# Optimization experiments

Measured on AMD Instinct MI355X. Metric: run time of the kernel, lower is better.

## Reference

```python
import jax, jax.numpy as jnp
import numpy as np


def setup_inputs() -> dict:
    key = jax.random.key(0)
    k1, k2, k3 = jax.random.split(key, 3)
    early = jax.random.normal(k1, (64, 1, 512, 512), dtype=jnp.float32)
    middle = jax.random.normal(k2, (64, 1, 256, 256), dtype=jnp.float32)
    deep = jax.random.normal(k3, (64, 1, 128, 128), dtype=jnp.float32)
    return {"early": early, "middle": middle, "deep": deep, "max_features": 500000}


def reference(early, middle, deep, max_features):
    # Concatenate all scores and find the threshold = (max_features)-th entry of
    # the descending sort, i.e. the (max_features+1)-th largest value.
    all_scores = jnp.concatenate([early.ravel(), middle.ravel(), deep.ravel()])
    n = all_scores.shape[0]
    if max_features >= n:
        thresh = jnp.asarray(0.0, dtype=all_scores.dtype)
    else:
        # top_k(k+1)[-1] == sort(descending)[k]; avoids a full sort.
        topk_vals, _ = jax.lax.top_k(all_scores, max_features + 1)
        thresh = topk_vals[-1]
    thresh = jax.lax.stop_gradient(thresh)
    early_out = jnp.where(early < thresh, jnp.zeros((), early.dtype), early)
    middle_out = jnp.where(middle < thresh, jnp.zeros((), middle.dtype), middle)
    deep_out = jnp.where(deep < thresh, jnp.zeros((), deep.dtype), deep)
    return (early_out, middle_out, deep_out)
```

## Files before the change

kernel.cpp:

```cpp
#include <hip/hip_runtime.h>

typedef float nfloat4 __attribute__((ext_vector_type(4)));

#define WS_CANDCNT 0
#define WS_B1      1
#define WS_K2      2
#define WS_PFX     3
#define WS_K3      4
#define H1_REP     32
#define H2_REP     8
#define WS_HIST1R  16
#define WS_HIST2R  (16 + H1_REP * 256)
#define WS_HIST3   (WS_HIST2R + H2_REP * 4096)
#define WS_ZEND    (WS_HIST3 + 4096)
#define WS_CAND    WS_ZEND

#define STASH 2048

__device__ __forceinline__ unsigned fkey(float f) {
  unsigned x = __float_as_uint(f);
  return x ^ ((x & 0x80000000u) ? 0xFFFFFFFFu : 0x80000000u);
}
__device__ __forceinline__ float unkey(unsigned u) {
  unsigned x = u ^ ((u & 0x80000000u) ? 0x80000000u : 0xFFFFFFFFu);
  return __uint_as_float(x);
}

__device__ __forceinline__ unsigned block_scan_incl(unsigned v, unsigned* sh4) {
  const int t = threadIdx.x;
  unsigned p = v;
#pragma unroll
  for (int off = 1; off < 64; off <<= 1) {
    unsigned y = __shfl_up(p, off);
    if ((t & 63) >= off) p += y;
  }
  if ((t & 63) == 63) sh4[t >> 6] = p;
  __syncthreads();
  unsigned wo = 0;
  for (int w = 0; w < (t >> 6); ++w) wo += sh4[w];
  __syncthreads();
  return p + wo;
}

__device__ __forceinline__ uint2 select_desc256(const unsigned* __restrict__ gh,
                                                unsigned k, unsigned* sh4, unsigned* sel2) {
  const int t = threadIdx.x;
  unsigned cnt = gh[255 - t];
  unsigned incl = block_scan_incl(cnt, sh4);
  unsigned excl = incl - cnt;
  if (excl < k && incl >= k) { sel2[0] = (unsigned)(255 - t); sel2[1] = k - excl; }
  __syncthreads();
  uint2 r; r.x = sel2[0]; r.y = sel2[1];
  __syncthreads();
  return r;
}

__device__ __forceinline__ uint2 select_desc4096(const unsigned* __restrict__ gh,
                                                 unsigned k, unsigned* sh4, unsigned* sel2) {
  const int t = threadIdx.x;
  unsigned loc[16]; unsigned s = 0;
  const int base = 4095 - t * 16;
#pragma unroll
  for (int j = 0; j < 16; ++j) { unsigned c = gh[base - j]; loc[j] = c; s += c; }
  unsigned incl = block_scan_incl(s, sh4);
  unsigned excl = incl - s;
  if (excl < k && incl >= k) {
    unsigned cum = excl; int j = 0;
    while (cum + loc[j] < k) { cum += loc[j]; ++j; }
    sel2[0] = (unsigned)(base - j); sel2[1] = k - cum;
  }
  __syncthreads();
  uint2 r; r.x = sel2[0]; r.y = sel2[1];
  __syncthreads();
  return r;
}

__global__ void zero_ws(unsigned* __restrict__ ws) {
  int i = blockIdx.x * blockDim.x + threadIdx.x;
  if (i < WS_ZEND) ws[i] = 0u;
}

__global__ void __launch_bounds__(1024) hist1_kernel(
    const float* __restrict__ e, const float* __restrict__ m,
    const float* __restrict__ d, int n0v, int n1v, int n2v,
    unsigned* __restrict__ ws) {
  __shared__ unsigned h[256 * 32];
  for (int i = threadIdx.x; i < 256 * 32; i += 1024) h[i] = 0u;
  __syncthreads();
  const unsigned sub = threadIdx.x & 31u;
  const int gid = blockIdx.x * 1024 + threadIdx.x;
  const int G = gridDim.x * 1024;

  auto acc1 = [&](float4 f) {
    atomicAdd(&h[((fkey(f.x) >> 24) << 5) | sub], 1u);
    atomicAdd(&h[((fkey(f.y) >> 24) << 5) | sub], 1u);
    atomicAdd(&h[((fkey(f.z) >> 24) << 5) | sub], 1u);
    atomicAdd(&h[((fkey(f.w) >> 24) << 5) | sub], 1u);
  };
  auto sweep = [&](const float* src, int nv) {
    const float4* a4 = (const float4*)src;
    int v = gid;
    for (; v + 3 * G < nv; v += 4 * G) {
      float4 f0 = a4[v]; float4 f1 = a4[v + G];
      float4 f2 = a4[v + 2 * G]; float4 f3 = a4[v + 3 * G];
      acc1(f0); acc1(f1); acc1(f2); acc1(f3);
    }
    for (; v < nv; v += G) acc1(a4[v]);
  };
  sweep(e, n0v); sweep(m, n1v); sweep(d, n2v);
  __syncthreads();
  const int t = threadIdx.x;
  if (t < 256) {
    unsigned s = 0;
#pragma unroll
    for (int j = 0; j < 32; ++j) s += h[(t << 5) + ((t + j) & 31)];
    if (s) atomicAdd(&ws[WS_HIST1R + (blockIdx.x & (H1_REP - 1)) * 256 + t], s);
  }
}

__global__ void __launch_bounds__(256) sel1_kernel(
    const int* __restrict__ maxf, unsigned* __restrict__ ws, long long n) {
  __shared__ unsigned h256[256];
  __shared__ unsigned sh4[4];
  __shared__ unsigned sel2[2];
  const int t = threadIdx.x;
  unsigned s = 0;
#pragma unroll
  for (int r = 0; r < H1_REP; ++r) s += ws[WS_HIST1R + r * 256 + t];
  h256[t] = s;
  __syncthreads();
  long long kk = (long long)maxf[0] + 1;
  if (kk > n) {
    if (t == 0) ws[WS_B1] = 0x80u;
    return;
  }
  uint2 r = select_desc256(h256, (unsigned)kk, sh4, sel2);
  if (t == 0) { ws[WS_B1] = r.x; ws[WS_K2] = r.y; }
}

__global__ void __launch_bounds__(1024) scatter_kernel(
    const float* __restrict__ e, const float* __restrict__ m, const float* __restrict__ d,
    float* __restrict__ out, unsigned* __restrict__ ws, unsigned cap,
    int e_blks, int m_blks) {
  const int t = threadIdx.x;
  const int bid = blockIdx.x;
  __shared__ float    sh_v[STASH];
  __shared__ unsigned sh_i[STASH];
  __shared__ unsigned sh_cnt;
  __shared__ unsigned sh_base;
  if (t == 0) sh_cnt = 0u;
  const unsigned b1 = ws[WS_B1];
  __syncthreads();
  const float4* in4;
  if (bid < e_blks)               in4 = (const float4*)e + (long long)bid * 2048;
  else if (bid < e_blks + m_blks) in4 = (const float4*)m + (long long)(bid - e_blks) * 2048;
  else                            in4 = (const float4*)d + (long long)(bid - e_blks - m_blks) * 2048;
  const int out_base_v = bid * 2048;
  nfloat4* out4 = (nfloat4*)out + out_base_v;
  float* gcV = (float*)(ws + WS_CAND);
  unsigned* gcI = ws + WS_CAND + cap;
  auto emit1 = [&](float4 f, int v) {
    unsigned kx = fkey(f.x), ky = fkey(f.y), kz = fkey(f.z), kw = fkey(f.w);
    nfloat4 o;
    o.x = ((kx >> 24) >= b1) ? f.x : 0.0f;
    o.y = ((ky >> 24) >= b1) ? f.y : 0.0f;
    o.z = ((kz >> 24) >= b1) ? f.z : 0.0f;
    o.w = ((kw >> 24) >= b1) ? f.w : 0.0f;
    __builtin_nontemporal_store(o, &out4[v]);
    unsigned ks[4] = {kx, ky, kz, kw};
    float fs[4] = {f.x, f.y, f.z, f.w};
#pragma unroll
    for (int cc = 0; cc < 4; ++cc) {
      if ((ks[cc] >> 24) == b1) {
        unsigned idx = (unsigned)(out_base_v + v) * 4u + (unsigned)cc;
        unsigned pos = atomicAdd(&sh_cnt, 1u);
        if (pos < STASH) { sh_v[pos] = fs[cc]; sh_i[pos] = idx; }
        else {
          unsigned g = atomicAdd(&ws[WS_CANDCNT], 1u);
          gcV[g] = fs[cc]; gcI[g] = idx;
        }
      }
    }
  };
  float4 f0 = in4[t];
  float4 f1 = in4[1024 + t];
  emit1(f0, t);
  emit1(f1, 1024 + t);
  __syncthreads();
  if (t == 0) {
    unsigned tot = sh_cnt < STASH ? sh_cnt : STASH;
    sh_base = tot ? atomicAdd(&ws[WS_CANDCNT], tot) : 0u;
    sh_cnt = tot;
  }
  __syncthreads();
  const unsigned tot = sh_cnt;
  const unsigned base = sh_base;
  for (unsigned i = t; i < tot; i += 1024) {
    gcV[base + i] = sh_v[i];
    gcI[base + i] = sh_i[i];
  }
}

__global__ void __launch_bounds__(256) candhist2_kernel(
    unsigned* __restrict__ ws, unsigned cap) {
  const int t = threadIdx.x;
  __shared__ unsigned sh_hist[4096];
  for (int i = t; i < 4096; i += 256) sh_hist[i] = 0u;
  __syncthreads();
  unsigned cnt = ws[WS_CANDCNT]; if (cnt > cap) cnt = cap;
  const float* candV = (const float*)(ws + WS_CAND);
  const unsigned G = gridDim.x * 256;
  for (unsigned i = blockIdx.x * 256 + t; i < cnt; i += G) {
    unsigned u = fkey(candV[i]);
    atomicAdd(&sh_hist[(u >> 12) & 0xFFFu], 1u);
  }
  __syncthreads();
  const unsigned rep = (blockIdx.x & (H2_REP - 1)) * 4096u;
  for (int i = t; i < 4096; i += 256) {
    unsigned v = sh_hist[i];
    if (v) atomicAdd(&ws[WS_HIST2R + rep + i], v);
  }
}

__global__ void __launch_bounds__(256) candhist3_kernel(
    const int* __restrict__ maxf, unsigned* __restrict__ ws, unsigned cap, long long n) {
  const int t = threadIdx.x;
  __shared__ unsigned sh_hist[4096];
  __shared__ unsigned sh4[4];
  __shared__ unsigned sel2[2];

  long long kk = (long long)maxf[0] + 1;
  unsigned pfx;
  if (kk > n) {
    pfx = 0x80u << 12;
  } else {
    for (int i = t; i < 4096; i += 256) {
      unsigned s = 0;
#pragma unroll
      for (int r = 0; r < H2_REP; ++r) s += ws[WS_HIST2R + r * 4096 + i];
      sh_hist[i] = s;
    }
    __syncthreads();
    unsigned b1 = ws[WS_B1];
    unsigned k2 = ws[WS_K2];
    uint2 r2 = select_desc4096(sh_hist, k2, sh4, sel2);
    pfx = (b1 << 12) | r2.x;
    if (blockIdx.x == 0 && t == 0) { ws[WS_PFX] = pfx; ws[WS_K3] = r2.y; }
    __syncthreads();
  }
  for (int i = t; i < 4096; i += 256) sh_hist[i] = 0u;
  __syncthreads();

  unsigned cnt = ws[WS_CANDCNT]; if (cnt > cap) cnt = cap;
  const float* candV = (const float*)(ws + WS_CAND);
  const unsigned G = gridDim.x * 256;
  for (unsigned i = blockIdx.x * 256 + t; i < cnt; i += G) {
    unsigned u = fkey(candV[i]);
    if ((u >> 12) == pfx) atomicAdd(&sh_hist[u & 0xFFFu], 1u);
  }
  __syncthreads();
  for (int i = t; i < 4096; i += 256) {
    unsigned v = sh_hist[i];
    if (v) atomicAdd(&ws[WS_HIST3 + i], v);
  }
}

__global__ void __launch_bounds__(256) fixup_kernel(
    float* __restrict__ out, const int* __restrict__ maxf,
    unsigned* __restrict__ ws, unsigned cap, long long n) {
  const int t = threadIdx.x;
  __shared__ unsigned sh4[4];
  __shared__ unsigned sel2[2];

  long long kk = (long long)maxf[0] + 1;
  float th;
  if (kk > n) {
    th = 0.0f;
    __syncthreads();
  } else {
    unsigned pfx = ws[WS_PFX];
    unsigned k3  = ws[WS_K3];
    uint2 r3 = select_desc4096(ws + WS_HIST3, k3, sh4, sel2);
    th = unkey((pfx << 12) | r3.x);
  }

  unsigned cnt = ws[WS_CANDCNT]; if (cnt > cap) cnt = cap;
  const float* candV = (const float*)(ws + WS_CAND);
  const unsigned* candI = ws + WS_CAND + cap;
  const unsigned G = gridDim.x * 256;
  for (unsigned i = blockIdx.x * 256 + t; i < cnt; i += G) {
    float f = candV[i];
    if (f < th) out[candI[i]] = 0.0f;
  }
}

extern "C" void kernel_launch(void* const* d_in, const int* in_sizes, int n_in,
                              void* d_out, int out_size, void* d_ws, size_t ws_size,
                              hipStream_t stream) {
  const float* e = (const float*)d_in[0];
  const float* m = (const float*)d_in[1];
  const float* d = (const float*)d_in[2];
  const int* maxf = (const int*)d_in[3];
  float* out = (float*)d_out;
  unsigned* ws = (unsigned*)d_ws;

  const long long n0 = in_sizes[0], n1 = in_sizes[1], n2 = in_sizes[2];
  const long long n = n0 + n1 + n2;
  const int n0v = (int)(n0 / 4), n1v = (int)(n1 / 4), n2v = (int)(n2 / 4);

  long long capll = ((long long)(ws_size / 4) - WS_CAND) / 2;
  if (capll < 0) capll = 0;
  if (capll > n) capll = n;
  const unsigned cap = (unsigned)capll;

  const int e_blks = (int)(n0 / 8192), m_blks = (int)(n1 / 8192);
  const int nblocks = (int)(n / 8192);

  zero_ws<<<(WS_ZEND + 255) / 256, 256, 0, stream>>>(ws);
  hist1_kernel<<<512, 1024, 0, stream>>>(e, m, d, n0v, n1v, n2v, ws);
  sel1_kernel<<<1, 256, 0, stream>>>(maxf, ws, n);
  scatter_kernel<<<nblocks, 1024, 0, stream>>>(e, m, d, out, ws, cap, e_blks, m_blks);
  candhist2_kernel<<<128, 256, 0, stream>>>(ws, cap);
  candhist3_kernel<<<128, 256, 0, stream>>>(maxf, ws, cap, n);
  fixup_kernel<<<256, 256, 0, stream>>>(out, maxf, ws, cap, n);
}
```

Baseline: 212.2 us.

## Use wave-ballot match aggregation for top-byte histogram with one block per tile

Replaces the grid-stride histogram with 32-way replicated shared bins by a fixed-tile kernel: each 1024-thread block loads 16384 floats and counts top-byte keys by matching equal keys across the wavefront with 8 ballots, so one lane per distinct key issues a single shared atomic. The intent is to cut LDS atomic contention and traffic, since Gaussian data concentrates in a few top-byte bins. The cost is extra ballot instructions per element and many more blocks (one per tile). It also assumes each input size is a multiple of 16384.

```diff
diff --git a/kernel.cpp b/kernel.cpp
--- a/kernel.cpp
+++ b/kernel.cpp
@@ -82,39 +82,47 @@
 
 __global__ void __launch_bounds__(1024) hist1_kernel(
     const float* __restrict__ e, const float* __restrict__ m,
-    const float* __restrict__ d, int n0v, int n1v, int n2v,
-    unsigned* __restrict__ ws) {
-  __shared__ unsigned h[256 * 32];
-  for (int i = threadIdx.x; i < 256 * 32; i += 1024) h[i] = 0u;
-  __syncthreads();
-  const unsigned sub = threadIdx.x & 31u;
-  const int gid = blockIdx.x * 1024 + threadIdx.x;
-  const int G = gridDim.x * 1024;
-
-  auto acc1 = [&](float4 f) {
-    atomicAdd(&h[((fkey(f.x) >> 24) << 5) | sub], 1u);
-    atomicAdd(&h[((fkey(f.y) >> 24) << 5) | sub], 1u);
-    atomicAdd(&h[((fkey(f.z) >> 24) << 5) | sub], 1u);
-    atomicAdd(&h[((fkey(f.w) >> 24) << 5) | sub], 1u);
+    const float* __restrict__ d, unsigned* __restrict__ ws,
+    int e_blks1, int m_blks1) {
+  __shared__ unsigned h[256];
+  const int t = threadIdx.x;
+  const int bid = blockIdx.x;
+  const int lane = t & 63;
+  if (t < 256) h[t] = 0u;
+  __syncthreads();
+
+  const float4* in4;
+  if (bid < e_blks1)                in4 = (const float4*)e + (long long)bid * 4096;
+  else if (bid < e_blks1 + m_blks1) in4 = (const float4*)m + (long long)(bid - e_blks1) * 4096;
+  else                              in4 = (const float4*)d + (long long)(bid - e_blks1 - m_blks1) * 4096;
+
+  float4 f0 = in4[t];
+  float4 f1 = in4[1024 + t];
+  float4 f2 = in4[2048 + t];
+  float4 f3 = in4[3072 + t];
+
+  auto count1 = [&](unsigned k) {
+    unsigned long long ms = __ballot(1);
+#pragma unroll
+    for (int b = 0; b < 8; ++b) {
+      unsigned long long bb = __ballot((k >> b) & 1u);
+      ms &= ((k >> b) & 1u) ? bb : ~bb;
+    }
+    if ((unsigned)__builtin_ctzll(ms) == (unsigned)lane)
+      atomicAdd(&h[k], (unsigned)__builtin_popcountll(ms));
   };
-  auto sweep = [&](const float* src, int nv) {
-    const float4* a4 = (const float4*)src;
-    int v = gid;
-    for (; v + 3 * G < nv; v += 4 * G) {
-      float4 f0 = a4[v]; float4 f1 = a4[v + G];
-      float4 f2 = a4[v + 2 * G]; float4 f3 = a4[v + 3 * G];
-      acc1(f0); acc1(f1); acc1(f2); acc1(f3);
-    }
-    for (; v < nv; v += G) acc1(a4[v]);
+  auto acc = [&](float4 f) {
+    count1(fkey(f.x) >> 24);
+    count1(fkey(f.y) >> 24);
+    count1(fkey(f.z) >> 24);
+    count1(fkey(f.w) >> 24);
   };
-  sweep(e, n0v); sweep(m, n1v); sweep(d, n2v);
-  __syncthreads();
-  const int t = threadIdx.x;
+  acc(f0); acc(f1); acc(f2); acc(f3);
+
+  __syncthreads();
   if (t < 256) {
-    unsigned s = 0;
-#pragma unroll
-    for (int j = 0; j < 32; ++j) s += h[(t << 5) + ((t + j) & 31)];
-    if (s) atomicAdd(&ws[WS_HIST1R + (blockIdx.x & (H1_REP - 1)) * 256 + t], s);
+    unsigned s = h[t];
+    if (s) atomicAdd(&ws[WS_HIST1R + (bid & (H1_REP - 1)) * 256 + t], s);
   }
 }
 
@@ -306,7 +314,6 @@
 
   const long long n0 = in_sizes[0], n1 = in_sizes[1], n2 = in_sizes[2];
   const long long n = n0 + n1 + n2;
-  const int n0v = (int)(n0 / 4), n1v = (int)(n1 / 4), n2v = (int)(n2 / 4);
 
   long long capll = ((long long)(ws_size / 4) - WS_CAND) / 2;
   if (capll < 0) capll = 0;
@@ -316,8 +323,11 @@
   const int e_blks = (int)(n0 / 8192), m_blks = (int)(n1 / 8192);
   const int nblocks = (int)(n / 8192);
 
+  const int e_blks1 = (int)(n0 / 16384), m_blks1 = (int)(n1 / 16384);
+  const int nblocks1 = (int)(n / 16384);
+
   zero_ws<<<(WS_ZEND + 255) / 256, 256, 0, stream>>>(ws);
-  hist1_kernel<<<512, 1024, 0, stream>>>(e, m, d, n0v, n1v, n2v, ws);
+  hist1_kernel<<<nblocks1, 1024, 0, stream>>>(e, m, d, ws, e_blks1, m_blks1);
   sel1_kernel<<<1, 256, 0, stream>>>(maxf, ws, n);
   scatter_kernel<<<nblocks, 1024, 0, stream>>>(e, m, d, out, ws, cap, e_blks, m_blks);
   candhist2_kernel<<<128, 256, 0, stream>>>(ws, cap);
```

Result: slower. 229.8 us (+8.3%).

## Split first radix histogram into two 16-bin register-counted passes

Applied to the files above, without the earlier changes.

Replaces the 256-bin shared-memory atomic histogram with two passes over the input. Each pass counts 16 bins in per-thread registers: first the top 4 key bits, then the next 4 bits within the selected nibble. Bucket selection moves into the heads of hist16b and scatter, which removes the single-block sel1 launch. This trades heavy LDS atomic contention for an extra full read of the inputs and 16 compares per element.

```diff
diff --git a/kernel.cpp b/kernel.cpp
--- a/kernel.cpp
+++ b/kernel.cpp
@@ -7,13 +7,14 @@
 #define WS_K2      2
 #define WS_PFX     3
 #define WS_K3      4
-#define H1_REP     32
+#define H16_REP    16
+#define WS_H16A    16
+#define WS_H16B    272
 #define H2_REP     8
-#define WS_HIST1R  16
-#define WS_HIST2R  (16 + H1_REP * 256)
-#define WS_HIST3   (WS_HIST2R + H2_REP * 4096)
-#define WS_ZEND    (WS_HIST3 + 4096)
-#define WS_CAND    WS_ZEND
+#define WS_HIST2R  528
+#define WS_HIST3   33296
+#define WS_ZEND    37392
+#define WS_CAND    37392
 
 #define STASH 2048
 
@@ -40,19 +41,6 @@
   for (int w = 0; w < (t >> 6); ++w) wo += sh4[w];
   __syncthreads();
   return p + wo;
-}
-
-__device__ __forceinline__ uint2 select_desc256(const unsigned* __restrict__ gh,
-                                                unsigned k, unsigned* sh4, unsigned* sel2) {
-  const int t = threadIdx.x;
-  unsigned cnt = gh[255 - t];
-  unsigned incl = block_scan_incl(cnt, sh4);
-  unsigned excl = incl - cnt;
-  if (excl < k && incl >= k) { sel2[0] = (unsigned)(255 - t); sel2[1] = k - excl; }
-  __syncthreads();
-  uint2 r; r.x = sel2[0]; r.y = sel2[1];
-  __syncthreads();
-  return r;
 }
 
 __device__ __forceinline__ uint2 select_desc4096(const unsigned* __restrict__ gh,
@@ -75,82 +63,169 @@
   return r;
 }
 
+__device__ __forceinline__ uint2 sel16_serial(const unsigned* h, unsigned k) {
+  unsigned cum = 0; int b = 15;
+  for (; b > 0; --b) {
+    if (cum + h[b] >= k) break;
+    cum += h[b];
+  }
+  uint2 r; r.x = (unsigned)b; r.y = k - cum;
+  return r;
+}
+
 __global__ void zero_ws(unsigned* __restrict__ ws) {
   int i = blockIdx.x * blockDim.x + threadIdx.x;
   if (i < WS_ZEND) ws[i] = 0u;
 }
 
-__global__ void __launch_bounds__(1024) hist1_kernel(
+__global__ void __launch_bounds__(1024) hist16a_kernel(
     const float* __restrict__ e, const float* __restrict__ m,
     const float* __restrict__ d, int n0v, int n1v, int n2v,
     unsigned* __restrict__ ws) {
-  __shared__ unsigned h[256 * 32];
-  for (int i = threadIdx.x; i < 256 * 32; i += 1024) h[i] = 0u;
-  __syncthreads();
-  const unsigned sub = threadIdx.x & 31u;
-  const int gid = blockIdx.x * 1024 + threadIdx.x;
+  __shared__ unsigned sh[16 * 32];
+  const int t = threadIdx.x;
+  for (int i = t; i < 16 * 32; i += 1024) sh[i] = 0u;
+  __syncthreads();
+
+  unsigned c[16];
+#pragma unroll
+  for (int i = 0; i < 16; ++i) c[i] = 0u;
+
+  const int gid = blockIdx.x * 1024 + t;
   const int G = gridDim.x * 1024;
 
-  auto acc1 = [&](float4 f) {
-    atomicAdd(&h[((fkey(f.x) >> 24) << 5) | sub], 1u);
-    atomicAdd(&h[((fkey(f.y) >> 24) << 5) | sub], 1u);
-    atomicAdd(&h[((fkey(f.z) >> 24) << 5) | sub], 1u);
-    atomicAdd(&h[((fkey(f.w) >> 24) << 5) | sub], 1u);
+  auto count1 = [&](float x) {
+    unsigned b = fkey(x) >> 28;
+#pragma unroll
+    for (int i = 0; i < 16; ++i) c[i] += (b == (unsigned)i) ? 1u : 0u;
   };
+  auto acc = [&](float4 f) { count1(f.x); count1(f.y); count1(f.z); count1(f.w); };
   auto sweep = [&](const float* src, int nv) {
     const float4* a4 = (const float4*)src;
     int v = gid;
     for (; v + 3 * G < nv; v += 4 * G) {
       float4 f0 = a4[v]; float4 f1 = a4[v + G];
       float4 f2 = a4[v + 2 * G]; float4 f3 = a4[v + 3 * G];
-      acc1(f0); acc1(f1); acc1(f2); acc1(f3);
+      acc(f0); acc(f1); acc(f2); acc(f3);
     }
-    for (; v < nv; v += G) acc1(a4[v]);
+    for (; v < nv; v += G) acc(a4[v]);
   };
   sweep(e, n0v); sweep(m, n1v); sweep(d, n2v);
-  __syncthreads();
-  const int t = threadIdx.x;
+
+  const int ln = t & 31;
+#pragma unroll
+  for (int i = 0; i < 16; ++i)
+    if (c[i]) atomicAdd(&sh[i * 32 + ln], c[i]);
+  __syncthreads();
+  if (t < 16) {
+    unsigned s = 0;
+#pragma unroll
+    for (int j = 0; j < 32; ++j) s += sh[t * 32 + j];
+    if (s) atomicAdd(&ws[WS_H16A + (blockIdx.x & (H16_REP - 1)) * 16 + t], s);
+  }
+}
+
+__global__ void __launch_bounds__(1024) hist16b_kernel(
+    const float* __restrict__ e, const float* __restrict__ m,
+    const float* __restrict__ d, int n0v, int n1v, int n2v,
+    unsigned* __restrict__ ws, const int* __restrict__ maxf, long long n) {
+  __shared__ unsigned sh[16 * 32];
+  __shared__ unsigned shc[16];
+  __shared__ unsigned sh_c1;
+  const int t = threadIdx.x;
+  for (int i = t; i < 16 * 32; i += 1024) sh[i] = 0u;
+  if (t < 16) shc[t] = 0u;
+  __syncthreads();
   if (t < 256) {
+    unsigned v = ws[WS_H16A + t];
+    if (v) atomicAdd(&shc[t & 15], v);
+  }
+  __syncthreads();
+  if (t == 0) {
+    long long kk = (long long)maxf[0] + 1;
+    if (kk > n) sh_c1 = 8u;
+    else        sh_c1 = sel16_serial(shc, (unsigned)kk).x;
+  }
+  __syncthreads();
+  const unsigned base8 = sh_c1 << 4;
+
+  unsigned c[16];
+#pragma unroll
+  for (int i = 0; i < 16; ++i) c[i] = 0u;
+
+  const int gid = blockIdx.x * 1024 + t;
+  const int G = gridDim.x * 1024;
+
+  auto count1 = [&](float x) {
+    unsigned f8 = fkey(x) >> 24;
+#pragma unroll
+    for (int i = 0; i < 16; ++i) c[i] += (f8 == base8 + (unsigned)i) ? 1u : 0u;
+  };
+  auto acc = [&](float4 f) { count1(f.x); count1(f.y); count1(f.z); count1(f.w); };
+  auto sweep = [&](const float* src, int nv) {
+    const float4* a4 = (const float4*)src;
+    int v = gid;
+    for (; v + 3 * G < nv; v += 4 * G) {
+      float4 f0 = a4[v]; float4 f1 = a4[v + G];
+      float4 f2 = a4[v + 2 * G]; float4 f3 = a4[v + 3 * G];
+      acc(f0); acc(f1); acc(f2); acc(f3);
+    }
+    for (; v < nv; v += G) acc(a4[v]);
+  };
+  sweep(e, n0v); sweep(m, n1v); sweep(d, n2v);
+
+  const int ln = t & 31;
+#pragma unroll
+  for (int i = 0; i < 16; ++i)
+    if (c[i]) atomicAdd(&sh[i * 32 + ln], c[i]);
+  __syncthreads();
+  if (t < 16) {
     unsigned s = 0;
 #pragma unroll
-    for (int j = 0; j < 32; ++j) s += h[(t << 5) + ((t + j) & 31)];
-    if (s) atomicAdd(&ws[WS_HIST1R + (blockIdx.x & (H1_REP - 1)) * 256 + t], s);
-  }
-}
-
-__global__ void __launch_bounds__(256) sel1_kernel(
-    const int* __restrict__ maxf, unsigned* __restrict__ ws, long long n) {
-  __shared__ unsigned h256[256];
-  __shared__ unsigned sh4[4];
-  __shared__ unsigned sel2[2];
-  const int t = threadIdx.x;
-  unsigned s = 0;
-#pragma unroll
-  for (int r = 0; r < H1_REP; ++r) s += ws[WS_HIST1R + r * 256 + t];
-  h256[t] = s;
-  __syncthreads();
-  long long kk = (long long)maxf[0] + 1;
-  if (kk > n) {
-    if (t == 0) ws[WS_B1] = 0x80u;
-    return;
-  }
-  uint2 r = select_desc256(h256, (unsigned)kk, sh4, sel2);
-  if (t == 0) { ws[WS_B1] = r.x; ws[WS_K2] = r.y; }
+    for (int j = 0; j < 32; ++j) s += sh[t * 32 + j];
+    if (s) atomicAdd(&ws[WS_H16B + (blockIdx.x & (H16_REP - 1)) * 16 + t], s);
+  }
 }
 
 __global__ void __launch_bounds__(1024) scatter_kernel(
     const float* __restrict__ e, const float* __restrict__ m, const float* __restrict__ d,
     float* __restrict__ out, unsigned* __restrict__ ws, unsigned cap,
-    int e_blks, int m_blks) {
+    int e_blks, int m_blks, const int* __restrict__ maxf, long long n) {
   const int t = threadIdx.x;
   const int bid = blockIdx.x;
   __shared__ float    sh_v[STASH];
   __shared__ unsigned sh_i[STASH];
+  __shared__ unsigned shc[16], shf[16];
   __shared__ unsigned sh_cnt;
   __shared__ unsigned sh_base;
+  __shared__ unsigned sh_b1;
   if (t == 0) sh_cnt = 0u;
-  const unsigned b1 = ws[WS_B1];
-  __syncthreads();
+  if (t < 16) { shc[t] = 0u; shf[t] = 0u; }
+  __syncthreads();
+  if (t < 256) {
+    unsigned v = ws[WS_H16A + t];
+    if (v) atomicAdd(&shc[t & 15], v);
+    unsigned w = ws[WS_H16B + t];
+    if (w) atomicAdd(&shf[t & 15], w);
+  }
+  __syncthreads();
+  if (t == 0) {
+    long long kk = (long long)maxf[0] + 1;
+    unsigned b1, k2o = 0;
+    if (kk > n) {
+      b1 = 0x80u;
+    } else {
+      uint2 r1 = sel16_serial(shc, (unsigned)kk);
+      uint2 r2 = sel16_serial(shf, r1.y);
+      b1 = (r1.x << 4) | r2.x;
+      k2o = r2.y;
+    }
+    sh_b1 = b1;
+    if (bid == 0) { ws[WS_B1] = b1; ws[WS_K2] = k2o; }
+  }
+  __syncthreads();
+  const unsigned b1 = sh_b1;
+
   const float4* in4;
   if (bid < e_blks)               in4 = (const float4*)e + (long long)bid * 2048;
   else if (bid < e_blks + m_blks) in4 = (const float4*)m + (long long)(bid - e_blks) * 2048;
@@ -317,9 +392,9 @@
   const int nblocks = (int)(n / 8192);
 
   zero_ws<<<(WS_ZEND + 255) / 256, 256, 0, stream>>>(ws);
-  hist1_kernel<<<512, 1024, 0, stream>>>(e, m, d, n0v, n1v, n2v, ws);
-  sel1_kernel<<<1, 256, 0, stream>>>(maxf, ws, n);
-  scatter_kernel<<<nblocks, 1024, 0, stream>>>(e, m, d, out, ws, cap, e_blks, m_blks);
+  hist16a_kernel<<<512, 1024, 0, stream>>>(e, m, d, n0v, n1v, n2v, ws);
+  hist16b_kernel<<<512, 1024, 0, stream>>>(e, m, d, n0v, n1v, n2v, ws, maxf, n);
+  scatter_kernel<<<nblocks, 1024, 0, stream>>>(e, m, d, out, ws, cap, e_blks, m_blks, maxf, n);
   candhist2_kernel<<<128, 256, 0, stream>>>(ws, cap);
   candhist3_kernel<<<128, 256, 0, stream>>>(maxf, ws, cap, n);
   fixup_kernel<<<256, 256, 0, stream>>>(out, maxf, ws, cap, n);
```

Result: slower. 312.9 us (+47.5%).
